# Performance work log

Measured on AMD Instinct MI355X. Metric: run time of the kernel, lower is better.

The kernel has to match this reference:

```python
import jax, jax.numpy as jnp
import numpy as np

L, D, H, F_IN = 3, 256, 8, 5
HD = D // H
FF = 4 * D
EPS = 1e-5


def _layer_norm(x, g, b):
    mu = jnp.mean(x, axis=-1, keepdims=True)
    var = jnp.mean(jnp.square(x - mu), axis=-1, keepdims=True)
    return (x - mu) * jax.lax.rsqrt(var + EPS) * g + b


def setup_inputs() -> dict:
    key = jax.random.key(0)
    ks = jax.random.split(key, 20)
    s = 0.02
    inp = {
        'x': jax.random.normal(ks[0], (32, 512, F_IN), jnp.float32),
        'mask': jax.random.randint(ks[1], (32, 512), 0, 2) == 1,
        'Win': jax.random.normal(ks[2], (F_IN, D), jnp.float32) * s,
        'bin_': jnp.zeros((D,), jnp.float32),
        'Wq': jax.random.normal(ks[3], (L, D, D), jnp.float32) * s,
        'bq': jnp.zeros((L, D), jnp.float32),
        'Wk': jax.random.normal(ks[4], (L, D, D), jnp.float32) * s,
        'bk': jnp.zeros((L, D), jnp.float32),
        'Wv': jax.random.normal(ks[5], (L, D, D), jnp.float32) * s,
        'bv': jnp.zeros((L, D), jnp.float32),
        'Wo': jax.random.normal(ks[6], (L, D, D), jnp.float32) * s,
        'bo': jnp.zeros((L, D), jnp.float32),
        'g1': jnp.ones((L, D), jnp.float32),
        'b1': jnp.zeros((L, D), jnp.float32),
        'W1': jax.random.normal(ks[7], (L, D, FF), jnp.float32) * s,
        'c1': jnp.zeros((L, FF), jnp.float32),
        'W2': jax.random.normal(ks[8], (L, FF, D), jnp.float32) * s,
        'c2': jnp.zeros((L, D), jnp.float32),
        'g2': jnp.ones((L, D), jnp.float32),
        'b2': jnp.zeros((L, D), jnp.float32),
    }
    return inp


def reference(x, mask, Win, bin_, Wq, bq, Wk, bk, Wv, bv, Wo, bo, g1, b1, W1, c1, W2, c2, g2, b2):
    B, S, _ = x.shape
    scale = 1.0 / jnp.sqrt(jnp.float32(HD))
    h = x @ Win + bin_  # [B,S,D]
    kmask = mask[:, None, None, :]  # [B,1,1,S] key-padding mask
    for l in range(L):
        q = (h @ Wq[l] + bq[l]).reshape(B, S, H, HD).transpose(0, 2, 1, 3)
        k = (h @ Wk[l] + bk[l]).reshape(B, S, H, HD).transpose(0, 2, 1, 3)
        v = (h @ Wv[l] + bv[l]).reshape(B, S, H, HD).transpose(0, 2, 1, 3)
        scores = jnp.einsum('bhqd,bhkd->bhqk', q, k) * scale
        scores = jnp.where(kmask, -jnp.inf, scores)
        attn = jnp.nan_to_num(jax.nn.softmax(scores, axis=-1), nan=0.0)
        ao = jnp.einsum('bhqk,bhkd->bhqd', attn, v).transpose(0, 2, 1, 3).reshape(B, S, D)
        ao = ao @ Wo[l] + bo[l]
        h = _layer_norm(h + ao, g1[l], b1[l])
        ff = jax.nn.relu(h @ W1[l] + c1[l]) @ W2[l] + c2[l]
        h = _layer_norm(h + ff, g2[l], b2[l])
    return h
```

## Files before the change

kernel.cpp:

```cpp
#include <hip/hip_runtime.h>
#include <cstdint>

#define NLAYER 3
#define DMODEL 256
#define NHEAD 8
#define HEADD 32
#define FFDIM 1024
#define BATCH 32
#define SEQ 512
#define MTOK (BATCH*SEQ)

typedef __attribute__((ext_vector_type(8))) __bf16 bf16x8;
typedef __attribute__((ext_vector_type(4))) __bf16 bf16x4;
typedef __attribute__((ext_vector_type(4))) float f32x4;
typedef __attribute__((ext_vector_type(16))) float f32x16;

typedef __attribute__((address_space(1))) const uint8_t ga_t;
typedef __attribute__((address_space(3))) uint8_t la_t;
__device__ __forceinline__ void gll16(const void* g, void* l) {
    __builtin_amdgcn_global_load_lds((ga_t*)g, (la_t*)l, 16, 0, 0);
}

__global__ __launch_bounds__(256)
void prep_kernel(const float* __restrict__ Wq, const float* __restrict__ Wk,
                 const float* __restrict__ Wv, const float* __restrict__ Wo,
                 const float* __restrict__ W1, const float* __restrict__ W2,
                 const float* __restrict__ bq, const float* __restrict__ bk,
                 const float* __restrict__ bv,
                 __bf16* __restrict__ wqkv, __bf16* __restrict__ wot,
                 __bf16* __restrict__ w1f, __bf16* __restrict__ w2f,
                 float* __restrict__ bqkv,
                 const float* __restrict__ x, const float* __restrict__ Win,
                 const float* __restrict__ bin, __bf16* __restrict__ h16)
{
    const int bid = blockIdx.x;
    const int tid = threadIdx.x;
    if (bid >= 2313) {
        const int m0 = (bid - 2313) * 8;
        const float bv_ = bin[tid];
#pragma unroll
        for (int p = 0; p < 8; ++p) {
            const int m = m0 + p;
            const float* xr = x + (size_t)m * 5;
            float acc = bv_;
#pragma unroll
            for (int k = 0; k < 5; ++k) acc += xr[k] * Win[k * DMODEL + tid];
            h16[(size_t)m * DMODEL + tid] = (__bf16)acc;
        }
        return;
    }
    if (bid >= 3 * 768) {
        int idx = (bid - 3 * 768) * 256 + tid;
        int l = idx / 768, j = idx % 768;
        float v = (j < 256) ? bq[l * 256 + j]
                : (j < 512) ? bk[l * 256 + j - 256]
                            : bv[l * 256 + j - 512];
        bqkv[idx] = v;
        return;
    }
    const int l = bid / 768;
    const int rr = bid % 768;
    __shared__ float tile[32][33];
    const int c = tid & 31, rbase = tid >> 5;

    if (rr < 256) {
        const float* src; __bf16* dst; int t;
        if (rr < 192) {
            int ty = rr >> 6; t = rr & 63;
            src = (ty == 0 ? Wq : ty == 1 ? Wk : Wv) + (size_t)l * 65536;
            dst = wqkv + (size_t)l * 768 * 256 + (size_t)ty * 65536;
        } else {
            t = rr - 192; src = Wo + (size_t)l * 65536; dst = wot + (size_t)l * 65536;
        }
        const int tk = t >> 3, tj = t & 7;
#pragma unroll
        for (int p = 0; p < 4; ++p) {
            int kr = rbase + p * 8;
            tile[kr][c] = src[(size_t)(tk * 32 + kr) * 256 + tj * 32 + c];
        }
        __syncthreads();
#pragma unroll
        for (int p = 0; p < 4; ++p) {
            int nr = rbase + p * 8;
            dst[(size_t)(tj * 32 + nr) * 256 + tk * 32 + c] = (__bf16)tile[c][nr];
        }
        return;
    }
    const float* src; __bf16* dst; int N, KT, t;
    if (rr < 512) { t = rr - 256; src = W1 + (size_t)l * 262144;
                    dst = w1f + (size_t)l * 262144; N = 1024; KT = 8; }
    else          { t = rr - 512; src = W2 + (size_t)l * 262144;
                    dst = w2f + (size_t)l * 262144; N = 256;  KT = 32; }
    const int tn = N >> 5;
    const int tk = t / tn, tj = t % tn;
#pragma unroll
    for (int p = 0; p < 4; ++p) {
        int kr = rbase + p * 8;
        tile[kr][c] = src[(size_t)(tk * 32 + kr) * N + tj * 32 + c];
    }
    __syncthreads();
    if (tid < 128) {
        const int l_n = tid >> 2, k8 = tid & 3;
        const int n = tj * 32 + l_n;
        bf16x8 v;
#pragma unroll
        for (int j = 0; j < 8; ++j) v[j] = (__bf16)tile[k8 * 8 + j][l_n];
        *(bf16x8*)(dst + ((size_t)((n >> 4) * KT + tk) * 64 + k8 * 16 + (n & 15)) * 8) = v;
    }
}

template<int RELU>
__global__ __launch_bounds__(256, 2)
void gemm_kernel(const __bf16* __restrict__ A, const __bf16* __restrict__ Bt,
                 const float* __restrict__ bias,
                 __bf16* __restrict__ C, int N)
{
    __shared__ __bf16 Bs[128 * 256];
    __shared__ __bf16 As[2][64 * 64];
    const int tid = threadIdx.x;
    const int m0 = blockIdx.x * 128;
    const int n0 = blockIdx.y * 128;
    const int lane = tid & 63;
    const int wave = tid >> 6;
    const int wm = (wave & 1) * 64;
    const int wn = (wave >> 1) * 64;
    const int fr = lane & 15;
    const int quad = lane >> 4;

    {
        const int rsub = lane >> 5;
#pragma unroll
        for (int c = 0; c < 16; ++c) {
            const int rl = wave * 32 + c * 2 + rsub;
            const int g = ((lane & 31) - 4 * rl) & 31;
            gll16(Bt + (size_t)(n0 + rl) * 256 + g * 8,
                  Bs + (wave * 32 + c * 2) * 256);
        }
    }
    const int arow8 = lane >> 3;
    const int apos = lane & 7;
#define STAGE_A(ks, buf)                                                      \
    {                                                                         \
        _Pragma("unroll")                                                     \
        for (int s_ = 0; s_ < 2; ++s_) {                                      \
            const int c_ = wave * 2 + s_;                                     \
            const int row_ = c_ * 8 + arow8;                                  \
            const int g_ = apos ^ (row_ & 7);                                 \
            gll16(A + (size_t)(m0 + row_ + 64 * (g_ >> 2)) * 256              \
                    + (ks) * 32 + (g_ & 3) * 8,                               \
                  &As[buf][c_ * 8 * 64]);                                     \
        }                                                                     \
    }
    STAGE_A(0, 0);
    __syncthreads();

    f32x4 acc[4][4];
#pragma unroll
    for (int i = 0; i < 4; ++i)
#pragma unroll
        for (int j = 0; j < 4; ++j)
#pragma unroll
            for (int r = 0; r < 4; ++r) acc[i][j][r] = 0.f;

    const int aposr = ((wave & 1) * 4 + quad) ^ (fr & 7);

#pragma unroll
    for (int ks = 0; ks < 8; ++ks) {
        if (ks < 7) STAGE_A(ks + 1, (ks + 1) & 1);
        const __bf16* Ab = As[ks & 1];
        bf16x8 af[4], bfr[4];
#pragma unroll
        for (int i = 0; i < 4; ++i) {
            const int row = i * 16 + fr;
            af[i] = *(const bf16x8*)(Ab + row * 64 + aposr * 8);
        }
#pragma unroll
        for (int j = 0; j < 4; ++j) {
            const int row = wn + j * 16 + fr;
            const int pos = (ks * 4 + quad + 4 * fr) & 31;
            bfr[j] = *(const bf16x8*)(Bs + row * 256 + pos * 8);
        }
#pragma unroll
        for (int i = 0; i < 4; ++i)
#pragma unroll
            for (int j = 0; j < 4; ++j)
                acc[i][j] = __builtin_amdgcn_mfma_f32_16x16x32_bf16(
                    af[i], bfr[j], acc[i][j], 0, 0, 0);
        __syncthreads();
    }
#undef STAGE_A

#pragma unroll
    for (int i = 0; i < 4; ++i) {
#pragma unroll
        for (int j = 0; j < 4; ++j) {
            const int gc = n0 + wn + j * 16 + fr;
            const float bv = bias[gc];
#pragma unroll
            for (int r = 0; r < 4; ++r) {
                const int gr = m0 + wm + i * 16 + quad * 4 + r;
                float v = acc[i][j][r] + bv;
                if (RELU) v = fmaxf(v, 0.f);
                C[(size_t)gr * N + gc] = (__bf16)v;
            }
        }
    }
}

template<int LAST>
__global__ __launch_bounds__(256, 4)
void gemm_ln_kernel(const __bf16* __restrict__ A, const __bf16* __restrict__ Bt,
                    const float* __restrict__ bias, const __bf16* __restrict__ res,
                    const float* __restrict__ g, const float* __restrict__ be,
                    __bf16* __restrict__ out16, float* __restrict__ out32, int K)
{
    __shared__ __bf16 As[32 * 64];
    __shared__ __bf16 Bs[256 * 64];
    __shared__ float red[32 * 8];
    const int tid = threadIdx.x;
    const int m0 = blockIdx.x * 32;
    const int lane = tid & 63;
    const int wave = tid >> 6;
    const int wn = wave * 64;
    const int fr = lane & 15;
    const int quad = lane >> 4;
    const int lr = lane >> 3;
    const int qg = (lane & 7) ^ lr;
    const int frs = fr & 7;

    const __bf16* Ab = A  + (size_t)(m0 + wave * 8 + lr) * K + qg * 8;
    const __bf16* Bb = Bt + (size_t)(wave * 64 + lr) * K + qg * 8;

    f32x4 acc[2][4];
#pragma unroll
    for (int i = 0; i < 2; ++i)
#pragma unroll
        for (int j = 0; j < 4; ++j)
#pragma unroll
            for (int r = 0; r < 4; ++r) acc[i][j][r] = 0.f;

    for (int k0 = 0; k0 < K; k0 += 64) {
        gll16(Ab + k0, As + wave * 512);
#pragma unroll
        for (int p = 0; p < 8; ++p)
            gll16(Bb + (size_t)p * 8 * K + k0, Bs + (wave * 8 + p) * 512);
        __syncthreads();
#pragma unroll
        for (int kk = 0; kk < 2; ++kk) {
            bf16x8 af[2], bfr[4];
#pragma unroll
            for (int i = 0; i < 2; ++i) {
                int row = i * 16 + fr;
                af[i] = *(const bf16x8*)(As + row * 64 + (((kk * 4 + quad) ^ frs) * 8));
            }
#pragma unroll
            for (int j = 0; j < 4; ++j) {
                int row = wn + j * 16 + fr;
                bfr[j] = *(const bf16x8*)(Bs + row * 64 + (((kk * 4 + quad) ^ frs) * 8));
            }
#pragma unroll
            for (int i = 0; i < 2; ++i)
#pragma unroll
                for (int j = 0; j < 4; ++j)
                    acc[i][j] = __builtin_amdgcn_mfma_f32_16x16x32_bf16(
                        af[i], bfr[j], acc[i][j], 0, 0, 0);
        }
        __syncthreads();
    }

    float bv[4];
#pragma unroll
    for (int j = 0; j < 4; ++j) bv[j] = bias[wn + j * 16 + fr];

#pragma unroll
    for (int i = 0; i < 2; ++i) {
#pragma unroll
        for (int r = 0; r < 4; ++r) {
            const int row = i * 16 + quad * 4 + r;
            float ps = 0.f, pq = 0.f;
#pragma unroll
            for (int j = 0; j < 4; ++j) {
                const int gc = wn + j * 16 + fr;
                float v = acc[i][j][r] + bv[j]
                        + (float)res[(size_t)(m0 + row) * DMODEL + gc];
                acc[i][j][r] = v;
                ps += v;
                pq += v * v;
            }
#pragma unroll
            for (int off = 1; off < 16; off <<= 1) {
                ps += __shfl_xor(ps, off, 64);
                pq += __shfl_xor(pq, off, 64);
            }
            if (fr == 0) {
                red[row * 8 + wave * 2]     = ps;
                red[row * 8 + wave * 2 + 1] = pq;
            }
        }
    }
    __syncthreads();

#pragma unroll
    for (int i = 0; i < 2; ++i) {
#pragma unroll
        for (int r = 0; r < 4; ++r) {
            const int row = i * 16 + quad * 4 + r;
            f32x4 a = *(const f32x4*)(red + row * 8);
            f32x4 b2 = *(const f32x4*)(red + row * 8 + 4);
            const float s  = a[0] + a[2] + b2[0] + b2[2];
            const float sq = a[1] + a[3] + b2[1] + b2[3];
            const float mu = s * (1.f / DMODEL);
            const float var = sq * (1.f / DMODEL) - mu * mu;
            const float rs = rsqrtf(var + 1e-5f);
#pragma unroll
            for (int j = 0; j < 4; ++j) {
                const int gc = wn + j * 16 + fr;
                float y = (acc[i][j][r] - mu) * rs * g[gc] + be[gc];
                if (LAST) out32[(size_t)(m0 + row) * DMODEL + gc] = y;
                else      out16[(size_t)(m0 + row) * DMODEL + gc] = (__bf16)y;
            }
        }
    }
}

template<int LAST>
__global__ __launch_bounds__(256, 3)
void ff_kernel(const __bf16* __restrict__ A, const __bf16* __restrict__ w1f,
               const float* __restrict__ c1, const __bf16* __restrict__ w2f,
               const float* __restrict__ c2, const __bf16* __restrict__ res,
               const float* __restrict__ g, const float* __restrict__ be,
               __bf16* __restrict__ out16, float* __restrict__ out32)
{
    __shared__ __attribute__((aligned(16))) __bf16 As[4][32 * 64];
    __shared__ __attribute__((aligned(16))) __bf16 P[32 * 136];
    __shared__ float c1s[1024];
    __shared__ float red[32 * 8];
    const int tid = threadIdx.x;
    const int lane = tid & 63;
    const int wave = tid >> 6;
    const int fr = lane & 15;
    const int quad = lane >> 4;
    const int m0 = blockIdx.x * 32;
    const int frs = fr & 7;

    {
        const int lr = lane >> 3, pos = lane & 7;
#pragma unroll
        for (int c4 = 0; c4 < 4; ++c4) {
            const int row = c4 * 8 + lr;
            const int gsw = pos ^ (row & 7);
            gll16(A + (size_t)(m0 + row) * 256 + wave * 64 + gsw * 8,
                  &As[wave][c4 * 8 * 64]);
        }
    }
    *(f32x4*)(c1s + tid * 4) = *(const f32x4*)(c1 + tid * 4);

    f32x4 acc2[2][4];
#pragma unroll
    for (int i = 0; i < 2; ++i)
#pragma unroll
        for (int j = 0; j < 4; ++j)
#pragma unroll
            for (int r = 0; r < 4; ++r) acc2[i][j][r] = 0.f;
    __syncthreads();

    for (int ch = 0; ch < 8; ++ch) {
        f32x4 acc1[2][2];
#pragma unroll
        for (int i = 0; i < 2; ++i)
#pragma unroll
            for (int j = 0; j < 2; ++j)
#pragma unroll
                for (int r = 0; r < 4; ++r) acc1[i][j][r] = 0.f;
#pragma unroll
        for (int ks = 0; ks < 8; ++ks) {
            bf16x8 af[2], bfr[2];
#pragma unroll
            for (int i = 0; i < 2; ++i)
                af[i] = *(const bf16x8*)(&As[ks >> 1][(i * 16 + fr) * 64
                         + ((((ks & 1) * 4 + quad) ^ frs) * 8)]);
#pragma unroll
            for (int j = 0; j < 2; ++j) {
                const int ntf = ch * 8 + wave * 2 + j;
                bfr[j] = *(const bf16x8*)(w1f + ((size_t)(ntf * 8 + ks) * 64 + lane) * 8);
            }
#pragma unroll
            for (int i = 0; i < 2; ++i)
#pragma unroll
                for (int j = 0; j < 2; ++j)
                    acc1[i][j] = __builtin_amdgcn_mfma_f32_16x16x32_bf16(
                        af[i], bfr[j], acc1[i][j], 0, 0, 0);
        }
#pragma unroll
        for (int j = 0; j < 2; ++j) {
            const float cb = c1s[ch * 128 + wave * 32 + j * 16 + fr];
#pragma unroll
            for (int i = 0; i < 2; ++i)
#pragma unroll
                for (int r = 0; r < 4; ++r) {
                    const int rowm = i * 16 + quad * 4 + r;
                    float v = fmaxf(acc1[i][j][r] + cb, 0.f);
                    P[rowm * 136 + wave * 32 + j * 16 + fr] = (__bf16)v;
                }
        }
        __syncthreads();
#pragma unroll
        for (int ks = 0; ks < 4; ++ks) {
            bf16x8 pf[2], wf[4];
#pragma unroll
            for (int i = 0; i < 2; ++i)
                pf[i] = *(const bf16x8*)(P + (i * 16 + fr) * 136 + ks * 32 + quad * 8);
#pragma unroll
            for (int j = 0; j < 4; ++j) {
                const int ntg = wave * 4 + j;
                const int kt = ch * 4 + ks;
                wf[j] = *(const bf16x8*)(w2f + ((size_t)(ntg * 32 + kt) * 64 + lane) * 8);
            }
#pragma unroll
            for (int i = 0; i < 2; ++i)
#pragma unroll
                for (int j = 0; j < 4; ++j)
                    acc2[i][j] = __builtin_amdgcn_mfma_f32_16x16x32_bf16(
                        pf[i], wf[j], acc2[i][j], 0, 0, 0);
        }
        __syncthreads();
    }

    const int wn = wave * 64;
    float bv[4];
#pragma unroll
    for (int j = 0; j < 4; ++j) bv[j] = c2[wn + j * 16 + fr];

#pragma unroll
    for (int i = 0; i < 2; ++i) {
#pragma unroll
        for (int r = 0; r < 4; ++r) {
            const int row = i * 16 + quad * 4 + r;
            float ps = 0.f, pq = 0.f;
#pragma unroll
            for (int j = 0; j < 4; ++j) {
                const int gc = wn + j * 16 + fr;
                float v = acc2[i][j][r] + bv[j]
                        + (float)res[(size_t)(m0 + row) * DMODEL + gc];
                acc2[i][j][r] = v;
                ps += v;
                pq += v * v;
            }
#pragma unroll
            for (int off = 1; off < 16; off <<= 1) {
                ps += __shfl_xor(ps, off, 64);
                pq += __shfl_xor(pq, off, 64);
            }
            if (fr == 0) {
                red[row * 8 + wave * 2]     = ps;
                red[row * 8 + wave * 2 + 1] = pq;
            }
        }
    }
    __syncthreads();

#pragma unroll
    for (int i = 0; i < 2; ++i) {
#pragma unroll
        for (int r = 0; r < 4; ++r) {
            const int row = i * 16 + quad * 4 + r;
            f32x4 a = *(const f32x4*)(red + row * 8);
            f32x4 b2 = *(const f32x4*)(red + row * 8 + 4);
            const float s  = a[0] + a[2] + b2[0] + b2[2];
            const float sq = a[1] + a[3] + b2[1] + b2[3];
            const float mu = s * (1.f / DMODEL);
            const float var = sq * (1.f / DMODEL) - mu * mu;
            const float rs = rsqrtf(var + 1e-5f);
#pragma unroll
            for (int j = 0; j < 4; ++j) {
                const int gc = wn + j * 16 + fr;
                float y = (acc2[i][j][r] - mu) * rs * g[gc] + be[gc];
                if (LAST) out32[(size_t)(m0 + row) * DMODEL + gc] = y;
                else      out16[(size_t)(m0 + row) * DMODEL + gc] = (__bf16)y;
            }
        }
    }
}

__global__ __launch_bounds__(1024)
void attn_kernel(const __bf16* __restrict__ qkv, const int* __restrict__ mask,
                 __bf16* __restrict__ ao)
{
    __shared__ __bf16 Ks[512 * 40];
    __shared__ __bf16 Vt[32 * 520];
    __shared__ __bf16 Pq[16 * 32 * 40];
    __shared__ float maskadd[512];

    const int b = blockIdx.x >> 3;
    const int h = blockIdx.x & 7;
    const int t = threadIdx.x;
    const int lane = t & 63;
    const int wave = t >> 6;
    const int cl = lane & 31;
    const int kh = lane >> 5;
    const float scale = 0.17677669529663687f;

    const size_t base = (size_t)b * SEQ * 768;

#pragma unroll
    for (int p = 0; p < 2; ++p) {
        int idx = p * 1024 + t;
        int key = idx >> 2, ch = idx & 3;
        bf16x8 kv = *(const bf16x8*)(qkv + base + (size_t)key * 768 + 256 + h * 32 + ch * 8);
        *(bf16x8*)(Ks + key * 40 + ch * 8) = kv;
        bf16x8 vv = *(const bf16x8*)(qkv + base + (size_t)key * 768 + 512 + h * 32 + ch * 8);
#pragma unroll
        for (int j = 0; j < 8; ++j) Vt[(ch * 8 + j) * 520 + key] = vv[j];
    }
    if (t < 512) maskadd[t] = mask[b * SEQ + t] ? -1e30f : 0.f;
    __syncthreads();

    const int q0 = wave * 32;
    const __bf16* qrow = qkv + base + (size_t)(q0 + cl) * 768 + h * 32;
    bf16x8 qf0 = *(const bf16x8*)(qrow + kh * 8);
    bf16x8 qf1 = *(const bf16x8*)(qrow + 16 + kh * 8);

    f32x16 oacc;
#pragma unroll
    for (int i = 0; i < 16; ++i) oacc[i] = 0.f;
    float lsum = 0.f;
    __bf16* Pw = Pq + wave * 32 * 40;

    for (int kt = 0; kt < SEQ; kt += 32) {
        bf16x8 kf0 = *(const bf16x8*)(Ks + (kt + cl) * 40 + kh * 8);
        bf16x8 kf1 = *(const bf16x8*)(Ks + (kt + cl) * 40 + 16 + kh * 8);
        f32x16 s;
#pragma unroll
        for (int i = 0; i < 16; ++i) s[i] = 0.f;
        s = __builtin_amdgcn_mfma_f32_32x32x16_bf16(kf0, qf0, s, 0, 0, 0);
        s = __builtin_amdgcn_mfma_f32_32x32x16_bf16(kf1, qf1, s, 0, 0, 0);
        float pv[16];
#pragma unroll
        for (int g = 0; g < 4; ++g) {
            f32x4 mv = *(const f32x4*)(maskadd + kt + 8 * g + 4 * kh);
#pragma unroll
            for (int r = 0; r < 4; ++r) {
                float e = __expf(s[g * 4 + r] * scale + mv[r]);
                pv[g * 4 + r] = e;
                lsum += e;
            }
        }
#pragma unroll
        for (int g = 0; g < 4; ++g) {
            bf16x4 pb;
#pragma unroll
            for (int r = 0; r < 4; ++r) pb[r] = (__bf16)pv[g * 4 + r];
            *(bf16x4*)(Pw + cl * 40 + 8 * g + 4 * kh) = pb;
        }
        bf16x8 pf0 = *(const bf16x8*)(Pw + cl * 40 + kh * 8);
        bf16x8 pf1 = *(const bf16x8*)(Pw + cl * 40 + 16 + kh * 8);
        bf16x8 vf0 = *(const bf16x8*)(Vt + cl * 520 + kt + kh * 8);
        bf16x8 vf1 = *(const bf16x8*)(Vt + cl * 520 + kt + 16 + kh * 8);
        oacc = __builtin_amdgcn_mfma_f32_32x32x16_bf16(vf0, pf0, oacc, 0, 0, 0);
        oacc = __builtin_amdgcn_mfma_f32_32x32x16_bf16(vf1, pf1, oacc, 0, 0, 0);
    }

    lsum += __shfl_xor(lsum, 32);
    const float inv = (lsum > 0.f) ? 1.f / lsum : 0.f;
    __bf16* orow = ao + (size_t)(b * SEQ + q0 + cl) * DMODEL + h * 32;
#pragma unroll
    for (int g = 0; g < 4; ++g) {
        bf16x4 w;
#pragma unroll
        for (int r = 0; r < 4; ++r) w[r] = (__bf16)(oacc[g * 4 + r] * inv);
        *(bf16x4*)(orow + 8 * g + 4 * kh) = w;
    }
}

extern "C" void kernel_launch(void* const* d_in, const int* in_sizes, int n_in,
                              void* d_out, int out_size, void* d_ws, size_t ws_size,
                              hipStream_t stream)
{
    const float* x   = (const float*)d_in[0];
    const int*   mask= (const int*)d_in[1];
    const float* Win = (const float*)d_in[2];
    const float* bin = (const float*)d_in[3];
    const float* Wq  = (const float*)d_in[4];
    const float* bq  = (const float*)d_in[5];
    const float* Wk  = (const float*)d_in[6];
    const float* bk  = (const float*)d_in[7];
    const float* Wv  = (const float*)d_in[8];
    const float* bv  = (const float*)d_in[9];
    const float* Wo  = (const float*)d_in[10];
    const float* bo  = (const float*)d_in[11];
    const float* g1  = (const float*)d_in[12];
    const float* b1  = (const float*)d_in[13];
    const float* W1  = (const float*)d_in[14];
    const float* c1  = (const float*)d_in[15];
    const float* W2  = (const float*)d_in[16];
    const float* c2  = (const float*)d_in[17];
    const float* g2  = (const float*)d_in[18];
    const float* b2  = (const float*)d_in[19];

    char* ws = (char*)d_ws;
    size_t off = 0;
    auto alloc = [&](size_t bytes) -> void* {
        void* p = ws + off;
        off += (bytes + 255) & ~(size_t)255;
        return p;
    };
    __bf16* hA   = (__bf16*)alloc((size_t)MTOK * 256 * 2);
    __bf16* hB   = (__bf16*)alloc((size_t)MTOK * 256 * 2);
    __bf16* qkv  = (__bf16*)alloc((size_t)MTOK * 768 * 2);
    __bf16* ao   = (__bf16*)alloc((size_t)MTOK * 256 * 2);
    __bf16* wqkv = (__bf16*)alloc((size_t)3 * 768 * 256 * 2);
    __bf16* wot  = (__bf16*)alloc((size_t)3 * 256 * 256 * 2);
    __bf16* w1f  = (__bf16*)alloc((size_t)3 * 1024 * 256 * 2);
    __bf16* w2f  = (__bf16*)alloc((size_t)3 * 256 * 1024 * 2);
    float*  bqkv = (float*)alloc((size_t)3 * 768 * 4);

    prep_kernel<<<dim3(2313 + MTOK / 8), dim3(256), 0, stream>>>(
        Wq, Wk, Wv, Wo, W1, W2, bq, bk, bv, wqkv, wot, w1f, w2f, bqkv,
        x, Win, bin, hA);

    for (int l = 0; l < NLAYER; ++l) {
        gemm_kernel<0><<<dim3(128, 6), dim3(256), 0, stream>>>(
            hA, wqkv + (size_t)l * 768 * 256, bqkv + l * 768, qkv, 768);
        attn_kernel<<<dim3(256), dim3(1024), 0, stream>>>(qkv, mask, ao);
        gemm_ln_kernel<0><<<dim3(MTOK / 32), dim3(256), 0, stream>>>(
            ao, wot + (size_t)l * 65536, bo + l * 256, hA,
            g1 + l * 256, b1 + l * 256, hB, nullptr, 256);
        if (l == 2) {
            ff_kernel<1><<<dim3(MTOK / 32), dim3(256), 0, stream>>>(
                hB, w1f + (size_t)l * 262144, c1 + l * 1024,
                w2f + (size_t)l * 262144, c2 + l * 256, hB,
                g2 + l * 256, b2 + l * 256, nullptr, (float*)d_out);
        } else {
            ff_kernel<0><<<dim3(MTOK / 32), dim3(256), 0, stream>>>(
                hB, w1f + (size_t)l * 262144, c1 + l * 1024,
                w2f + (size_t)l * 262144, c2 + l * 256, hB,
                g2 + l * 256, b2 + l * 256, hA, nullptr);
        }
    }
}
```

Baseline: 359.7 us.

## Fuse QKV projection into attention kernel per batch-head block

Removes the separate QKV GEMM kernel. Each attention block (one batch, one head) now computes its own Q, K and V slices directly from the hidden states, using MFMA with per-head weights pre-packed into fragment order by the prep kernel. This drops the write and re-read of the large qkv intermediate and one launch per layer. The cost is that hidden-state rows are read from global memory once per head (8 times), and the shared memory and registers in the attention kernel grow.

```diff
diff --git a/kernel.cpp b/kernel.cpp
--- a/kernel.cpp
+++ b/kernel.cpp
@@ -27,7 +27,7 @@
                  const float* __restrict__ W1, const float* __restrict__ W2,
                  const float* __restrict__ bq, const float* __restrict__ bk,
                  const float* __restrict__ bv,
-                 __bf16* __restrict__ wqkv, __bf16* __restrict__ wot,
+                 __bf16* __restrict__ wqf, __bf16* __restrict__ wot,
                  __bf16* __restrict__ w1f, __bf16* __restrict__ w2f,
                  float* __restrict__ bqkv,
                  const float* __restrict__ x, const float* __restrict__ Win,
@@ -63,15 +63,32 @@
     __shared__ float tile[32][33];
     const int c = tid & 31, rbase = tid >> 5;
 
+    if (rr < 192) {
+        const int ty = rr >> 6;
+        const int t = rr & 63;
+        const float* src = (ty == 0 ? Wq : ty == 1 ? Wk : Wv) + (size_t)l * 65536;
+        const int tk = t >> 3, tj = t & 7;
+#pragma unroll
+        for (int p = 0; p < 4; ++p) {
+            int kr = rbase + p * 8;
+            tile[kr][c] = src[(size_t)(tk * 32 + kr) * 256 + tj * 32 + c];
+        }
+        __syncthreads();
+        if (tid < 128) {
+            const int lane = tid & 63, ksl = tid >> 6;
+            const int cl = lane & 31, kh = lane >> 5;
+            bf16x8 v;
+#pragma unroll
+            for (int j = 0; j < 8; ++j) v[j] = (__bf16)tile[ksl * 16 + kh * 8 + j][cl];
+            *(bf16x8*)(wqf + ((size_t)(((l * 8 + tj) * 3 + ty) * 16
+                              + tk * 2 + ksl)) * 512 + lane * 8) = v;
+        }
+        return;
+    }
     if (rr < 256) {
-        const float* src; __bf16* dst; int t;
-        if (rr < 192) {
-            int ty = rr >> 6; t = rr & 63;
-            src = (ty == 0 ? Wq : ty == 1 ? Wk : Wv) + (size_t)l * 65536;
-            dst = wqkv + (size_t)l * 768 * 256 + (size_t)ty * 65536;
-        } else {
-            t = rr - 192; src = Wo + (size_t)l * 65536; dst = wot + (size_t)l * 65536;
-        }
+        const int t = rr - 192;
+        const float* src = Wo + (size_t)l * 65536;
+        __bf16* dst = wot + (size_t)l * 65536;
         const int tk = t >> 3, tj = t & 7;
 #pragma unroll
         for (int p = 0; p < 4; ++p) {
@@ -109,101 +126,117 @@
     }
 }
 
-template<int RELU>
-__global__ __launch_bounds__(256, 2)
-void gemm_kernel(const __bf16* __restrict__ A, const __bf16* __restrict__ Bt,
-                 const float* __restrict__ bias,
-                 __bf16* __restrict__ C, int N)
+__global__ __launch_bounds__(1024)
+void attn_kernel(const __bf16* __restrict__ hA, const __bf16* __restrict__ wqf,
+                 const float* __restrict__ bqkv, const int* __restrict__ mask,
+                 __bf16* __restrict__ ao)
 {
-    __shared__ __bf16 Bs[128 * 256];
-    __shared__ __bf16 As[2][64 * 64];
-    const int tid = threadIdx.x;
-    const int m0 = blockIdx.x * 128;
-    const int n0 = blockIdx.y * 128;
-    const int lane = tid & 63;
-    const int wave = tid >> 6;
-    const int wm = (wave & 1) * 64;
-    const int wn = (wave >> 1) * 64;
-    const int fr = lane & 15;
-    const int quad = lane >> 4;
+    __shared__ __bf16 Ks[512 * 40];
+    __shared__ __bf16 Vt[32 * 520];
+    __shared__ __attribute__((aligned(16))) __bf16 Un[3*16*512];
+    __shared__ float maskadd[512];
+
+    const int b = blockIdx.x >> 3;
+    const int h = blockIdx.x & 7;
+    const int t = threadIdx.x;
+    const int lane = t & 63;
+    const int wave = t >> 6;
+    const int cl = lane & 31;
+    const int kh = lane >> 5;
+    const float scale = 0.17677669529663687f;
 
     {
-        const int rsub = lane >> 5;
-#pragma unroll
-        for (int c = 0; c < 16; ++c) {
-            const int rl = wave * 32 + c * 2 + rsub;
-            const int g = ((lane & 31) - 4 * rl) & 31;
-            gll16(Bt + (size_t)(n0 + rl) * 256 + g * 8,
-                  Bs + (wave * 32 + c * 2) * 256);
-        }
-    }
-    const int arow8 = lane >> 3;
-    const int apos = lane & 7;
-#define STAGE_A(ks, buf)                                                      \
-    {                                                                         \
-        _Pragma("unroll")                                                     \
-        for (int s_ = 0; s_ < 2; ++s_) {                                      \
-            const int c_ = wave * 2 + s_;                                     \
-            const int row_ = c_ * 8 + arow8;                                  \
-            const int g_ = apos ^ (row_ & 7);                                 \
-            gll16(A + (size_t)(m0 + row_ + 64 * (g_ >> 2)) * 256              \
-                    + (ks) * 32 + (g_ & 3) * 8,                               \
-                  &As[buf][c_ * 8 * 64]);                                     \
-        }                                                                     \
-    }
-    STAGE_A(0, 0);
-    __syncthreads();
-
-    f32x4 acc[4][4];
-#pragma unroll
-    for (int i = 0; i < 4; ++i)
-#pragma unroll
-        for (int j = 0; j < 4; ++j)
-#pragma unroll
-            for (int r = 0; r < 4; ++r) acc[i][j][r] = 0.f;
-
-    const int aposr = ((wave & 1) * 4 + quad) ^ (fr & 7);
-
-#pragma unroll
-    for (int ks = 0; ks < 8; ++ks) {
-        if (ks < 7) STAGE_A(ks + 1, (ks + 1) & 1);
-        const __bf16* Ab = As[ks & 1];
-        bf16x8 af[4], bfr[4];
-#pragma unroll
-        for (int i = 0; i < 4; ++i) {
-            const int row = i * 16 + fr;
-            af[i] = *(const bf16x8*)(Ab + row * 64 + aposr * 8);
-        }
-#pragma unroll
-        for (int j = 0; j < 4; ++j) {
-            const int row = wn + j * 16 + fr;
-            const int pos = (ks * 4 + quad + 4 * fr) & 31;
-            bfr[j] = *(const bf16x8*)(Bs + row * 256 + pos * 8);
-        }
-#pragma unroll
-        for (int i = 0; i < 4; ++i)
-#pragma unroll
-            for (int j = 0; j < 4; ++j)
-                acc[i][j] = __builtin_amdgcn_mfma_f32_16x16x32_bf16(
-                    af[i], bfr[j], acc[i][j], 0, 0, 0);
-        __syncthreads();
-    }
-#undef STAGE_A
-
-#pragma unroll
-    for (int i = 0; i < 4; ++i) {
-#pragma unroll
-        for (int j = 0; j < 4; ++j) {
-            const int gc = n0 + wn + j * 16 + fr;
-            const float bv = bias[gc];
+        const __bf16* wsrc = wqf + (size_t)h * 24576;
+#pragma unroll
+        for (int p = 0; p < 3; ++p) {
+            const int chunk = p * 1024 + t;
+            gll16(wsrc + (size_t)chunk * 8, Un + (p * 1024 + wave * 64) * 8);
+        }
+    }
+    if (t < 512) maskadd[t] = mask[b * SEQ + t] ? -1e30f : 0.f;
+    __syncthreads();
+
+    const int tok0 = wave * 32;
+    const size_t arow = ((size_t)(b * SEQ + tok0 + cl)) * 256;
+    f32x16 aQ, aK, aV;
+#pragma unroll
+    for (int i = 0; i < 16; ++i) { aQ[i] = 0.f; aK[i] = 0.f; aV[i] = 0.f; }
+#pragma unroll
+    for (int ks = 0; ks < 16; ++ks) {
+        bf16x8 tf = *(const bf16x8*)(hA + arow + ks * 16 + kh * 8);
+        bf16x8 wq = *(const bf16x8*)(Un + (0 * 16 + ks) * 512 + lane * 8);
+        bf16x8 wk = *(const bf16x8*)(Un + (1 * 16 + ks) * 512 + lane * 8);
+        bf16x8 wv = *(const bf16x8*)(Un + (2 * 16 + ks) * 512 + lane * 8);
+        aQ = __builtin_amdgcn_mfma_f32_32x32x16_bf16(wq, tf, aQ, 0, 0, 0);
+        aK = __builtin_amdgcn_mfma_f32_32x32x16_bf16(wk, tf, aK, 0, 0, 0);
+        aV = __builtin_amdgcn_mfma_f32_32x32x16_bf16(wv, tf, aV, 0, 0, 0);
+    }
+#pragma unroll
+    for (int r = 0; r < 16; ++r) {
+        const int rdim = (r & 3) + 8 * (r >> 2) + 4 * kh;
+        Ks[(tok0 + cl) * 40 + rdim] = (__bf16)(aK[r] + bqkv[256 + h * 32 + rdim]);
+        Vt[rdim * 520 + tok0 + cl]  = (__bf16)(aV[r] + bqkv[512 + h * 32 + rdim]);
+    }
+    __syncthreads();
+
+    __bf16* Pw = Un + wave * 1024;
+#pragma unroll
+    for (int r = 0; r < 16; ++r) {
+        const int rdim = (r & 3) + 8 * (r >> 2) + 4 * kh;
+        Pw[cl * 32 + rdim] = (__bf16)(aQ[r] + bqkv[h * 32 + rdim]);
+    }
+    bf16x8 qf0 = *(const bf16x8*)(Pw + cl * 32 + kh * 8);
+    bf16x8 qf1 = *(const bf16x8*)(Pw + cl * 32 + 16 + kh * 8);
+    __syncthreads();
+
+    f32x16 oacc;
+#pragma unroll
+    for (int i = 0; i < 16; ++i) oacc[i] = 0.f;
+    float lsum = 0.f;
+
+    for (int kt = 0; kt < SEQ; kt += 32) {
+        bf16x8 kf0 = *(const bf16x8*)(Ks + (kt + cl) * 40 + kh * 8);
+        bf16x8 kf1 = *(const bf16x8*)(Ks + (kt + cl) * 40 + 16 + kh * 8);
+        f32x16 s;
+#pragma unroll
+        for (int i = 0; i < 16; ++i) s[i] = 0.f;
+        s = __builtin_amdgcn_mfma_f32_32x32x16_bf16(kf0, qf0, s, 0, 0, 0);
+        s = __builtin_amdgcn_mfma_f32_32x32x16_bf16(kf1, qf1, s, 0, 0, 0);
+        float pv[16];
+#pragma unroll
+        for (int g = 0; g < 4; ++g) {
+            f32x4 mv = *(const f32x4*)(maskadd + kt + 8 * g + 4 * kh);
 #pragma unroll
             for (int r = 0; r < 4; ++r) {
-                const int gr = m0 + wm + i * 16 + quad * 4 + r;
-                float v = acc[i][j][r] + bv;
-                if (RELU) v = fmaxf(v, 0.f);
-                C[(size_t)gr * N + gc] = (__bf16)v;
-            }
-        }
+                float e = __expf(s[g * 4 + r] * scale + mv[r]);
+                pv[g * 4 + r] = e;
+                lsum += e;
+            }
+        }
+#pragma unroll
+        for (int g = 0; g < 4; ++g) {
+            bf16x4 pb;
+#pragma unroll
+            for (int r = 0; r < 4; ++r) pb[r] = (__bf16)pv[g * 4 + r];
+            *(bf16x4*)(Pw + cl * 32 + 8 * g + 4 * kh) = pb;
+        }
+        bf16x8 pf0 = *(const bf16x8*)(Pw + cl * 32 + kh * 8);
+        bf16x8 pf1 = *(const bf16x8*)(Pw + cl * 32 + 16 + kh * 8);
+        bf16x8 vf0 = *(const bf16x8*)(Vt + cl * 520 + kt + kh * 8);
+        bf16x8 vf1 = *(const bf16x8*)(Vt + cl * 520 + kt + 16 + kh * 8);
+        oacc = __builtin_amdgcn_mfma_f32_32x32x16_bf16(vf0, pf0, oacc, 0, 0, 0);
+        oacc = __builtin_amdgcn_mfma_f32_32x32x16_bf16(vf1, pf1, oacc, 0, 0, 0);
+    }
+
+    lsum += __shfl_xor(lsum, 32);
+    const float inv = (lsum > 0.f) ? 1.f / lsum : 0.f;
+    __bf16* orow = ao + (size_t)(b * SEQ + tok0 + cl) * DMODEL + h * 32;
+#pragma unroll
+    for (int g = 0; g < 4; ++g) {
+        bf16x4 w;
+#pragma unroll
+        for (int r = 0; r < 4; ++r) w[r] = (__bf16)(oacc[g * 4 + r] * inv);
+        *(bf16x4*)(orow + 8 * g + 4 * kh) = w;
     }
 }
 
@@ -479,96 +512,6 @@
                 else      out16[(size_t)(m0 + row) * DMODEL + gc] = (__bf16)y;
             }
         }
-    }
-}
-
-__global__ __launch_bounds__(1024)
-void attn_kernel(const __bf16* __restrict__ qkv, const int* __restrict__ mask,
-                 __bf16* __restrict__ ao)
-{
-    __shared__ __bf16 Ks[512 * 40];
-    __shared__ __bf16 Vt[32 * 520];
-    __shared__ __bf16 Pq[16 * 32 * 40];
-    __shared__ float maskadd[512];
-
-    const int b = blockIdx.x >> 3;
-    const int h = blockIdx.x & 7;
-    const int t = threadIdx.x;
-    const int lane = t & 63;
-    const int wave = t >> 6;
-    const int cl = lane & 31;
-    const int kh = lane >> 5;
-    const float scale = 0.17677669529663687f;
-
-    const size_t base = (size_t)b * SEQ * 768;
-
-#pragma unroll
-    for (int p = 0; p < 2; ++p) {
-        int idx = p * 1024 + t;
-        int key = idx >> 2, ch = idx & 3;
-        bf16x8 kv = *(const bf16x8*)(qkv + base + (size_t)key * 768 + 256 + h * 32 + ch * 8);
-        *(bf16x8*)(Ks + key * 40 + ch * 8) = kv;
-        bf16x8 vv = *(const bf16x8*)(qkv + base + (size_t)key * 768 + 512 + h * 32 + ch * 8);
-#pragma unroll
-        for (int j = 0; j < 8; ++j) Vt[(ch * 8 + j) * 520 + key] = vv[j];
-    }
-    if (t < 512) maskadd[t] = mask[b * SEQ + t] ? -1e30f : 0.f;
-    __syncthreads();
-
-    const int q0 = wave * 32;
-    const __bf16* qrow = qkv + base + (size_t)(q0 + cl) * 768 + h * 32;
-    bf16x8 qf0 = *(const bf16x8*)(qrow + kh * 8);
-    bf16x8 qf1 = *(const bf16x8*)(qrow + 16 + kh * 8);
-
-    f32x16 oacc;
-#pragma unroll
-    for (int i = 0; i < 16; ++i) oacc[i] = 0.f;
-    float lsum = 0.f;
-    __bf16* Pw = Pq + wave * 32 * 40;
-
-    for (int kt = 0; kt < SEQ; kt += 32) {
-        bf16x8 kf0 = *(const bf16x8*)(Ks + (kt + cl) * 40 + kh * 8);
-        bf16x8 kf1 = *(const bf16x8*)(Ks + (kt + cl) * 40 + 16 + kh * 8);
-        f32x16 s;
-#pragma unroll
-        for (int i = 0; i < 16; ++i) s[i] = 0.f;
-        s = __builtin_amdgcn_mfma_f32_32x32x16_bf16(kf0, qf0, s, 0, 0, 0);
-        s = __builtin_amdgcn_mfma_f32_32x32x16_bf16(kf1, qf1, s, 0, 0, 0);
-        float pv[16];
-#pragma unroll
-        for (int g = 0; g < 4; ++g) {
-            f32x4 mv = *(const f32x4*)(maskadd + kt + 8 * g + 4 * kh);
-#pragma unroll
-            for (int r = 0; r < 4; ++r) {
-                float e = __expf(s[g * 4 + r] * scale + mv[r]);
-                pv[g * 4 + r] = e;
-                lsum += e;
-            }
-        }
-#pragma unroll
-        for (int g = 0; g < 4; ++g) {
-            bf16x4 pb;
-#pragma unroll
-            for (int r = 0; r < 4; ++r) pb[r] = (__bf16)pv[g * 4 + r];
-            *(bf16x4*)(Pw + cl * 40 + 8 * g + 4 * kh) = pb;
-        }
-        bf16x8 pf0 = *(const bf16x8*)(Pw + cl * 40 + kh * 8);
-        bf16x8 pf1 = *(const bf16x8*)(Pw + cl * 40 + 16 + kh * 8);
-        bf16x8 vf0 = *(const bf16x8*)(Vt + cl * 520 + kt + kh * 8);
-        bf16x8 vf1 = *(const bf16x8*)(Vt + cl * 520 + kt + 16 + kh * 8);
-        oacc = __builtin_amdgcn_mfma_f32_32x32x16_bf16(vf0, pf0, oacc, 0, 0, 0);
-        oacc = __builtin_amdgcn_mfma_f32_32x32x16_bf16(vf1, pf1, oacc, 0, 0, 0);
-    }
-
-    lsum += __shfl_xor(lsum, 32);
-    const float inv = (lsum > 0.f) ? 1.f / lsum : 0.f;
-    __bf16* orow = ao + (size_t)(b * SEQ + q0 + cl) * DMODEL + h * 32;
-#pragma unroll
-    for (int g = 0; g < 4; ++g) {
-        bf16x4 w;
-#pragma unroll
-        for (int r = 0; r < 4; ++r) w[r] = (__bf16)(oacc[g * 4 + r] * inv);
-        *(bf16x4*)(orow + 8 * g + 4 * kh) = w;
     }
 }
 
@@ -606,22 +549,20 @@
     };
     __bf16* hA   = (__bf16*)alloc((size_t)MTOK * 256 * 2);
     __bf16* hB   = (__bf16*)alloc((size_t)MTOK * 256 * 2);
-    __bf16* qkv  = (__bf16*)alloc((size_t)MTOK * 768 * 2);
     __bf16* ao   = (__bf16*)alloc((size_t)MTOK * 256 * 2);
-    __bf16* wqkv = (__bf16*)alloc((size_t)3 * 768 * 256 * 2);
+    __bf16* wqf  = (__bf16*)alloc((size_t)3 * 8 * 3 * 16 * 512 * 2);
     __bf16* wot  = (__bf16*)alloc((size_t)3 * 256 * 256 * 2);
     __bf16* w1f  = (__bf16*)alloc((size_t)3 * 1024 * 256 * 2);
     __bf16* w2f  = (__bf16*)alloc((size_t)3 * 256 * 1024 * 2);
     float*  bqkv = (float*)alloc((size_t)3 * 768 * 4);
 
     prep_kernel<<<dim3(2313 + MTOK / 8), dim3(256), 0, stream>>>(
-        Wq, Wk, Wv, Wo, W1, W2, bq, bk, bv, wqkv, wot, w1f, w2f, bqkv,
+        Wq, Wk, Wv, Wo, W1, W2, bq, bk, bv, wqf, wot, w1f, w2f, bqkv,
         x, Win, bin, hA);
 
     for (int l = 0; l < NLAYER; ++l) {
-        gemm_kernel<0><<<dim3(128, 6), dim3(256), 0, stream>>>(
-            hA, wqkv + (size_t)l * 768 * 256, bqkv + l * 768, qkv, 768);
-        attn_kernel<<<dim3(256), dim3(1024), 0, stream>>>(qkv, mask, ao);
+        attn_kernel<<<dim3(256), dim3(1024), 0, stream>>>(
+            hA, wqf + (size_t)l * 8 * 3 * 16 * 512, bqkv + l * 768, mask, ao);
         gemm_ln_kernel<0><<<dim3(MTOK / 32), dim3(256), 0, stream>>>(
             ao, wot + (size_t)l * 65536, bo + l * 256, hA,
             g1 + l * 256, b1 + l * 256, hB, nullptr, 256);
```

Measured after the change: 364.9 us. Within noise of the previous version (+1.5%).
